# Kernel tuning notes

Measured on AMD Instinct MI355X. Metric: run time of the kernel, lower is better.

## Reference

```python
import jax, jax.numpy as jnp
import numpy as np
import math

GAUSSIAN_KERNEL = 3.0  # sigma from init_kwargs


def setup_inputs() -> dict:
    key = jax.random.key(0)
    k1, k2, k3, k4 = jax.random.split(key, 4)
    B, De, Do, T, H, W = 4, 128, 512, 10, 32, 32
    return {
        "m_in": jax.random.normal(k1, (B, De, T, H, W), dtype=jnp.float32),
        "m_out": jax.random.normal(k2, (B, Do, T, H, W), dtype=jnp.float32),
        "q_in": jax.random.normal(k3, (B, De, H, W), dtype=jnp.float32),
        "q_out": jax.random.normal(k4, (B, Do, H, W), dtype=jnp.float32),
    }


def _gaussian_kernel_map(corr, H, W, sigma):
    # corr: [B, THW, HW]; for each memory location, gaussian centered at its
    # argmax query position over the HxW query grid.
    idx = jnp.argmax(corr, axis=2)                       # [B, THW] int
    idx_y = (idx // W).astype(corr.dtype)[..., None, None]  # [B, THW, 1, 1]
    idx_x = (idx % W).astype(corr.dtype)[..., None, None]
    y = jnp.arange(H, dtype=corr.dtype).reshape(1, 1, H, 1)
    x = jnp.arange(W, dtype=corr.dtype).reshape(1, 1, 1, W)
    g = jnp.exp(-((x - idx_x) ** 2 + (y - idx_y) ** 2) / (2.0 * sigma ** 2))
    return g.reshape(corr.shape)                         # [B, THW, HW]


def reference(m_in, m_out, q_in, q_out):
    B, De, T, H, W = m_in.shape
    Do = m_out.shape[1]
    THW, HW = T * H * W, H * W

    mi = m_in.reshape(B, De, THW)       # [B, De, THW]
    qi = q_in.reshape(B, De, HW)        # [B, De, HW]
    # p[b, t, q] = <memory key t, query key q> / sqrt(De)
    p = jnp.einsum('bdt,bdq->btq', mi, qi) / math.sqrt(De)   # [B, THW, HW]

    gauss = _gaussian_kernel_map(p, H, W, GAUSSIAN_KERNEL)

    # softmax over memory dimension (dim=1), then gaussian reweight + renorm
    p_soft = jax.nn.softmax(p, axis=1)
    p_w = p_soft * gauss
    p_w = p_w / jnp.sum(p_w, axis=1, keepdims=True)

    mo = m_out.reshape(B, Do, THW)
    mem = jnp.einsum('bdt,btq->bdq', mo, p_w).reshape(B, Do, H, W)
    mem_out = jnp.concatenate([mem, q_out], axis=1)      # [B, 2*Do, H, W]
    return mem_out, p_w
```

## Files before the change

### kernel.cpp

```cpp
#include <hip/hip_runtime.h>
#include <hip/hip_bf16.h>

#define BB 4
#define DE 128
#define DO_ 512
#define THW 10240
#define HW 1024
#define SCALE 0.08838834764831845f
#define INV2S2 0.05555555555555555f
#define NCH 32
#define CHT 320

#define WS_PART_F  81920
#define WS_STATS_F 344064
#define WS_MO16_B  1409024ull
#define WS_PWT_B   43352064ull

using bf16x8 = __attribute__((ext_vector_type(8))) short;
using f32x4  = __attribute__((ext_vector_type(4))) float;
using u16x8  = __attribute__((ext_vector_type(8))) unsigned short;

__device__ __forceinline__ unsigned short f2bf(float f) {
    __hip_bfloat16 h = __float2bfloat16(f);
    return *reinterpret_cast<unsigned short*>(&h);
}
__device__ __forceinline__ void glds16(const void* g, void* l) {
    __builtin_amdgcn_global_load_lds((const __attribute__((address_space(1))) void*)g,
                                     (__attribute__((address_space(3))) void*)l,
                                     16, 0, 0);
}
__device__ __forceinline__ unsigned int ordf(float f) {
    unsigned int u = __float_as_uint(f);
    return (u & 0x80000000u) ? ~u : (u | 0x80000000u);
}

__global__ __launch_bounds__(256) void k_init(float* __restrict__ out,
                                              const float* __restrict__ qout,
                                              float4* __restrict__ amax4)
{
    int idx = blockIdx.x * 256 + threadIdx.x;
    if (idx < 20480) amax4[idx] = make_float4(0.f, 0.f, 0.f, 0.f);
    int b  = idx >> 18;
    int r  = idx & 262143;
    int c  = r >> 8;
    int q4 = r & 255;
    float4* dst = (float4*)out + idx;
    if (c < DO_) {
        *dst = make_float4(0.f, 0.f, 0.f, 0.f);
    } else {
        const float4* src = (const float4*)qout + ((size_t)(b * DO_ + (c - DO_)) << 8) + q4;
        *dst = *src;
    }
}

__global__ __launch_bounds__(256) void k_gemm1(const float* __restrict__ mi,
                                               const float* __restrict__ qi,
                                               float* __restrict__ p,
                                               unsigned long long* __restrict__ amax)
{
    __shared__ float As[32][128];
    __shared__ float Bs[32][128];
    int id  = blockIdx.x;
    int tbg = id & 7;
    int rr  = id >> 3;
    int b   = rr / 80;
    int j   = rr - b * 80;
    int tb  = tbg * 10 + (j >> 3);
    int qb  = j & 7;
    int tid = threadIdx.x;
    int tx = tid & 15, ty = tid >> 4;
    int lane = tid & 63;

    const float* A  = mi + (size_t)b * DE * THW + (size_t)tb * 128;
    const float* Bq = qi + (size_t)b * DE * HW  + qb * 128;

    float acc[8][8] = {};
    for (int kc = 0; kc < 4; ++kc) {
        __syncthreads();
#pragma unroll
        for (int i = 0; i < 4; ++i) {
            int s  = tid + i * 256;
            int kl = s >> 5;
            int c4 = (s & 31) << 2;
            *(float4*)&As[kl][c4] = *(const float4*)&A [(size_t)(kc * 32 + kl) * THW + c4];
            *(float4*)&Bs[kl][c4] = *(const float4*)&Bq[(size_t)(kc * 32 + kl) * HW  + c4];
        }
        __syncthreads();
#pragma unroll 2
        for (int kl = 0; kl < 32; ++kl) {
            float4 a0 = *(float4*)&As[kl][ty * 8];
            float4 a1 = *(float4*)&As[kl][ty * 8 + 4];
            float4 b0 = *(float4*)&Bs[kl][tx * 8];
            float4 b1 = *(float4*)&Bs[kl][tx * 8 + 4];
            float av[8] = {a0.x, a0.y, a0.z, a0.w, a1.x, a1.y, a1.z, a1.w};
            float bv[8] = {b0.x, b0.y, b0.z, b0.w, b1.x, b1.y, b1.z, b1.w};
#pragma unroll
            for (int i2 = 0; i2 < 8; ++i2)
#pragma unroll
                for (int j2 = 0; j2 < 8; ++j2)
                    acc[i2][j2] = fmaf(av[i2], bv[j2], acc[i2][j2]);
        }
    }

    size_t rowbase = ((size_t)b * THW + (size_t)tb * 128 + ty * 8) * HW + qb * 128 + tx * 8;
    int q0 = qb * 128 + tx * 8;
#pragma unroll
    for (int i = 0; i < 8; ++i) {
        float v[8];
#pragma unroll
        for (int j2 = 0; j2 < 8; ++j2) v[j2] = acc[i][j2] * SCALE;
        *(float4*)&p[rowbase + (size_t)i * HW]     = make_float4(v[0], v[1], v[2], v[3]);
        *(float4*)&p[rowbase + (size_t)i * HW + 4] = make_float4(v[4], v[5], v[6], v[7]);
        float best = v[0]; int bq = q0;
#pragma unroll
        for (int j2 = 1; j2 < 8; ++j2)
            if (v[j2] > best) { best = v[j2]; bq = q0 + j2; }
        unsigned long long pk = ((unsigned long long)ordf(best) << 32)
                              | (unsigned long long)(0xFFFFFFFFu - (unsigned)bq);
#pragma unroll
        for (int off = 1; off < 16; off <<= 1) {
            unsigned long long o = __shfl_xor(pk, off);
            if (o > pk) pk = o;
        }
        if ((lane & 15) == 0)
            atomicMax(&amax[(size_t)b * THW + (size_t)tb * 128 + ty * 8 + i], pk);
    }
}

__global__ __launch_bounds__(256) void k_colstats(const float* __restrict__ p,
                                                  const unsigned long long* __restrict__ amax,
                                                  float* __restrict__ part)
{
    int q  = blockIdx.x * 256 + threadIdx.x;
    int ch = blockIdx.y, b = blockIdx.z;
    float x = (float)(q & 31), y = (float)(q >> 5);
    const float* pp = p + ((size_t)b * THW + ch * CHT) * HW + q;
    const unsigned long long* am = amax + (size_t)b * THW + ch * CHT;
    float m = -3.0e38f, s = 0.f;
    for (int i = 0; i < CHT; ++i) {
        unsigned idx = 0xFFFFFFFFu - (unsigned)am[i];
        float dx = x - (float)(idx & 31), dy = y - (float)(idx >> 5);
        float z = pp[(size_t)i * HW] - (dx * dx + dy * dy) * INV2S2;
        float nm = fmaxf(m, z);
        s = s * __expf(m - nm) + __expf(z - nm);
        m = nm;
    }
    size_t o = ((size_t)(b * NCH + ch) * HW + q) * 2;
    part[o] = m; part[o + 1] = s;
}

__global__ __launch_bounds__(256) void k_reduce(const float* __restrict__ part,
                                                float* __restrict__ stats)
{
    int i = blockIdx.x * 256 + threadIdx.x;
    int b = i >> 10, q = i & 1023;
    float M = -3.0e38f;
#pragma unroll
    for (int c = 0; c < NCH; ++c)
        M = fmaxf(M, part[((size_t)(b * NCH + c) * HW + q) * 2]);
    float S = 0.f;
#pragma unroll
    for (int c = 0; c < NCH; ++c) {
        size_t o = ((size_t)(b * NCH + c) * HW + q) * 2;
        S += part[o + 1] * __expf(part[o] - M);
    }
    stats[(size_t)i * 2] = M;
    stats[(size_t)i * 2 + 1] = 1.0f / S;
}

__global__ __launch_bounds__(256) void k_pwt(float* __restrict__ p,
                                             const unsigned long long* __restrict__ amax,
                                             const float* __restrict__ stats,
                                             unsigned short* __restrict__ pwT)
{
    __shared__ float tile[64][65];
    __shared__ float ctr[128];
    __shared__ float st[128];
    int qb = blockIdx.x, tb = blockIdx.y, b = blockIdx.z;
    int tid = threadIdx.x;
    if (tid < 64) {
        unsigned idx = 0xFFFFFFFFu - (unsigned)amax[(size_t)b * THW + tb * 64 + tid];
        ctr[tid * 2]     = (float)(idx & 31);
        ctr[tid * 2 + 1] = (float)(idx >> 5);
    }
    if (tid < 128)
        st[tid] = stats[((size_t)b * HW + qb * 64) * 2 + tid];
    __syncthreads();
    int r0 = tid >> 4;
    int c4 = (tid & 15) << 2;
#pragma unroll
    for (int i = 0; i < 4; ++i) {
        int r = r0 + i * 16;
        float* pp = p + ((size_t)b * THW + tb * 64 + r) * HW + qb * 64 + c4;
        float4 v = *(float4*)pp;
        float cx = ctr[r * 2], cy = ctr[r * 2 + 1];
        float vv[4] = {v.x, v.y, v.z, v.w};
#pragma unroll
        for (int j = 0; j < 4; ++j) {
            int q = qb * 64 + c4 + j;
            float x = (float)(q & 31), y = (float)(q >> 5);
            float dx = x - cx, dy = y - cy;
            vv[j] = __expf(vv[j] - (dx * dx + dy * dy) * INV2S2 - st[(c4 + j) * 2])
                    * st[(c4 + j) * 2 + 1];
            tile[r][c4 + j] = vv[j];
        }
        *(float4*)pp = make_float4(vv[0], vv[1], vv[2], vv[3]);
    }
    __syncthreads();
    int ql = tid >> 3;
    int t0 = (tid & 7) << 3;
#pragma unroll
    for (int pass = 0; pass < 2; ++pass) {
        int q = ql + pass * 32;
        u16x8 o8;
#pragma unroll
        for (int j = 0; j < 8; ++j)
            o8[j] = f2bf(tile[t0 + j][q]);
        *(u16x8*)&pwT[((size_t)b * HW + qb * 64 + q) * THW + tb * 64 + t0] = o8;
    }
}

__global__ __launch_bounds__(256) void k_mo16(const float* __restrict__ mo,
                                              unsigned short* __restrict__ o)
{
    size_t base = ((size_t)blockIdx.x * 256 + threadIdx.x) * 8;
    float4 a = *(const float4*)(mo + base);
    float4 c = *(const float4*)(mo + base + 4);
    u16x8 v;
    v[0] = f2bf(a.x); v[1] = f2bf(a.y); v[2] = f2bf(a.z); v[3] = f2bf(a.w);
    v[4] = f2bf(c.x); v[5] = f2bf(c.y); v[6] = f2bf(c.z); v[7] = f2bf(c.w);
    *(u16x8*)(o + base) = v;
}

__global__ __launch_bounds__(256) void k_gemm2m(const unsigned short* __restrict__ A16,
                                                const unsigned short* __restrict__ B16,
                                                float* __restrict__ out)
{
    __shared__ unsigned short As[4096];
    __shared__ unsigned short Bs[4096];
    int id   = blockIdx.x;
    int xcd  = id & 7;
    int rest = id >> 3;
    int shi  = rest >> 5;
    int jj   = rest & 31;
    int s    = xcd + (shi << 3);
    int b    = s >> 2, ks = s & 3;
    int mb   = jj >> 3, nb = jj & 7;
    int tid = threadIdx.x;
    int w = tid >> 6, lane = tid & 63;
    int quad = lane >> 4, l15 = lane & 15;

    const char* Ag = (const char*)(A16 + (size_t)b * DO_ * THW + (size_t)mb * 128 * THW + ks * 2560);
    const char* Bg = (const char*)(B16 + (size_t)b * HW * THW + (size_t)nb * 128 * THW + ks * 2560);

    int srow = lane >> 2;
    int sj   = (lane & 3) ^ (srow & 3);
    const char* aP0 = Ag + (size_t)((w * 2 + 0) * 16 + srow) * (THW * 2) + sj * 16;
    const char* aP1 = Ag + (size_t)((w * 2 + 1) * 16 + srow) * (THW * 2) + sj * 16;
    const char* bP0 = Bg + (size_t)((w * 2 + 0) * 16 + srow) * (THW * 2) + sj * 16;
    const char* bP1 = Bg + (size_t)((w * 2 + 1) * 16 + srow) * (THW * 2) + sj * 16;
    char* lA0 = (char*)As + (w * 2 + 0) * 1024;
    char* lA1 = (char*)As + (w * 2 + 1) * 1024;
    char* lB0 = (char*)Bs + (w * 2 + 0) * 1024;
    char* lB1 = (char*)Bs + (w * 2 + 1) * 1024;

    int wm = w >> 1, wn = w & 1;
    int fq = ((l15 & 3) ^ quad) << 4;
    const char* aF = (const char*)As + (wm * 64 + l15) * 64 + fq;
    const char* bF = (const char*)Bs + (wn * 64 + l15) * 64 + fq;

    f32x4 acc[4][4];
#pragma unroll
    for (int i = 0; i < 4; ++i)
#pragma unroll
        for (int j = 0; j < 4; ++j)
            acc[i][j] = (f32x4){0.f, 0.f, 0.f, 0.f};

    for (int kit = 0; kit < 80; ++kit) {
        int kb = kit * 64;
        __syncthreads();
        glds16(aP0 + kb, lA0);
        glds16(aP1 + kb, lA1);
        glds16(bP0 + kb, lB0);
        glds16(bP1 + kb, lB1);
        __syncthreads();
        bf16x8 af[4], bfr[4];
#pragma unroll
        for (int i = 0; i < 4; ++i) af[i]  = *(const bf16x8*)(aF + i * 1024);
#pragma unroll
        for (int j = 0; j < 4; ++j) bfr[j] = *(const bf16x8*)(bF + j * 1024);
#pragma unroll
        for (int i = 0; i < 4; ++i)
#pragma unroll
            for (int j = 0; j < 4; ++j)
                acc[i][j] = __builtin_amdgcn_mfma_f32_16x16x32_bf16(af[i], bfr[j], acc[i][j], 0, 0, 0);
    }

    float* Cg = out + (size_t)b * (2 * DO_ * HW);
    int d0 = mb * 128 + wm * 64 + quad * 4;
    int q0 = nb * 128 + wn * 64 + l15;
#pragma unroll
    for (int i = 0; i < 4; ++i)
#pragma unroll
        for (int j = 0; j < 4; ++j)
#pragma unroll
            for (int r = 0; r < 4; ++r)
                atomicAdd(&Cg[(size_t)(d0 + i * 16 + r) * HW + q0 + j * 16], acc[i][j][r]);
}

extern "C" void kernel_launch(void* const* d_in, const int* in_sizes, int n_in,
                              void* d_out, int out_size, void* d_ws, size_t ws_size,
                              hipStream_t stream)
{
    const float* m_in  = (const float*)d_in[0];
    const float* m_out = (const float*)d_in[1];
    const float* q_in  = (const float*)d_in[2];
    const float* q_out = (const float*)d_in[3];
    float* out = (float*)d_out;
    float* pw  = out + (size_t)BB * 2 * DO_ * HW;
    float* ws  = (float*)d_ws;
    unsigned long long* amax = (unsigned long long*)d_ws;
    float* part    = ws + WS_PART_F;
    float* stats   = ws + WS_STATS_F;
    unsigned short* mo16  = (unsigned short*)((char*)d_ws + WS_MO16_B);
    unsigned short* pwT16 = (unsigned short*)((char*)d_ws + WS_PWT_B);

    hipLaunchKernelGGL(k_init,    dim3(4096),        dim3(256), 0, stream, out, q_out, (float4*)d_ws);
    hipLaunchKernelGGL(k_mo16,    dim3(10240),       dim3(256), 0, stream, m_out, mo16);
    hipLaunchKernelGGL(k_gemm1,   dim3(2560),        dim3(256), 0, stream, m_in, q_in, pw, amax);
    hipLaunchKernelGGL(k_colstats,dim3(4, NCH, BB),  dim3(256), 0, stream, pw, amax, part);
    hipLaunchKernelGGL(k_reduce,  dim3(16),          dim3(256), 0, stream, part, stats);
    hipLaunchKernelGGL(k_pwt,     dim3(16, 160, BB), dim3(256), 0, stream, pw, amax, stats, pwT16);
    hipLaunchKernelGGL(k_gemm2m,  dim3(512),         dim3(256), 0, stream, mo16, pwT16, out);
}
```

Measured before the change: 576.4 us.

## Run first GEMM on fp16 MFMA with hi/lo split for fp32 accuracy

Replaces the scalar fp32 FMA GEMM for the key correlation with an MFMA fp16 GEMM. The inputs are first split into high and low fp16 parts, transposed to a K-contiguous layout, and the query scale is folded in. Three MFMA products (HH, HL, LH) approximate fp32 accuracy, and LDS is filled with global_load_lds and XOR swizzling. The split buffers reuse the pwT16 workspace region, so the mo16 conversion launch is moved after the stats kernels. The cost is extra conversion passes and some precision risk near argmax ties.

```diff
diff --git a/kernel.cpp b/kernel.cpp
--- a/kernel.cpp
+++ b/kernel.cpp
@@ -15,8 +15,13 @@
 #define WS_STATS_F 344064
 #define WS_MO16_B  1409024ull
 #define WS_PWT_B   43352064ull
+#define WS_MITH_B  (WS_PWT_B)
+#define WS_MITL_B  (WS_PWT_B + 10485760ull)
+#define WS_QITH_B  (WS_PWT_B + 20971520ull)
+#define WS_QITL_B  (WS_PWT_B + 22020096ull)
 
 using bf16x8 = __attribute__((ext_vector_type(8))) short;
+using f16x8  = __attribute__((ext_vector_type(8))) _Float16;
 using f32x4  = __attribute__((ext_vector_type(4))) float;
 using u16x8  = __attribute__((ext_vector_type(8))) unsigned short;
 
@@ -53,13 +58,56 @@
     }
 }
 
-__global__ __launch_bounds__(256) void k_gemm1(const float* __restrict__ mi,
-                                               const float* __restrict__ qi,
-                                               float* __restrict__ p,
-                                               unsigned long long* __restrict__ amax)
-{
-    __shared__ float As[32][128];
-    __shared__ float Bs[32][128];
+__global__ __launch_bounds__(256) void k_split(const float* __restrict__ src,
+                                               unsigned short* __restrict__ dstH,
+                                               unsigned short* __restrict__ dstL,
+                                               int ncols, float scale)
+{
+    __shared__ float tile[128][65];
+    int t0 = blockIdx.x * 64;
+    int b  = blockIdx.z;
+    int tid = threadIdx.x;
+    const float* S = src + (size_t)b * DE * ncols + t0;
+#pragma unroll
+    for (int i = 0; i < 8; ++i) {
+        int s  = tid + i * 256;
+        int k  = s >> 4;
+        int c4 = (s & 15) << 2;
+        *(float4*)&tile[k][c4] = *(const float4*)&S[(size_t)k * ncols + c4];
+    }
+    __syncthreads();
+#pragma unroll
+    for (int i = 0; i < 4; ++i) {
+        int s  = tid + i * 256;
+        int t  = s >> 4;
+        int k8 = s & 15;
+        u16x8 oh, ol;
+#pragma unroll
+        for (int j = 0; j < 8; ++j) {
+            float v = tile[k8 * 8 + j][t] * scale;
+            _Float16 h = (_Float16)v;
+            float rr = v - (float)h;
+            _Float16 l = (_Float16)(rr * 2048.0f);
+            oh[j] = *(unsigned short*)&h;
+            ol[j] = *(unsigned short*)&l;
+        }
+        size_t o = ((size_t)b * ncols + t0 + t) * 128 + k8 * 8;
+        *(u16x8*)&dstH[o] = oh;
+        *(u16x8*)&dstL[o] = ol;
+    }
+}
+
+__global__ __launch_bounds__(256) void k_gemm1m(const unsigned short* __restrict__ AH,
+                                                const unsigned short* __restrict__ AL,
+                                                const unsigned short* __restrict__ BH,
+                                                const unsigned short* __restrict__ BL,
+                                                float* __restrict__ p,
+                                                unsigned long long* __restrict__ amax)
+{
+    __shared__ unsigned short AsH[4096];
+    __shared__ unsigned short AsL[4096];
+    __shared__ unsigned short BsH[4096];
+    __shared__ unsigned short BsL[4096];
     int id  = blockIdx.x;
     int tbg = id & 7;
     int rr  = id >> 3;
@@ -68,62 +116,102 @@
     int tb  = tbg * 10 + (j >> 3);
     int qb  = j & 7;
     int tid = threadIdx.x;
-    int tx = tid & 15, ty = tid >> 4;
-    int lane = tid & 63;
-
-    const float* A  = mi + (size_t)b * DE * THW + (size_t)tb * 128;
-    const float* Bq = qi + (size_t)b * DE * HW  + qb * 128;
-
-    float acc[8][8] = {};
+    int w = tid >> 6, lane = tid & 63;
+    int quad = lane >> 4, l15 = lane & 15;
+
+    const char* AgH = (const char*)AH + ((size_t)b * THW + (size_t)tb * 128) * 256;
+    const char* AgL = (const char*)AL + ((size_t)b * THW + (size_t)tb * 128) * 256;
+    const char* BgH = (const char*)BH + ((size_t)b * HW + qb * 128) * 256;
+    const char* BgL = (const char*)BL + ((size_t)b * HW + qb * 128) * 256;
+
+    int srow = lane >> 2;
+    int sj   = (lane & 3) ^ (srow & 3);
+    size_t ro0 = (size_t)(w * 32 + srow) * 256 + sj * 16;
+    size_t ro1 = (size_t)(w * 32 + 16 + srow) * 256 + sj * 16;
+    char* lds0[4] = {(char*)AsH + w * 2048, (char*)AsL + w * 2048,
+                     (char*)BsH + w * 2048, (char*)BsL + w * 2048};
+    const char* gl0[4] = {AgH, AgL, BgH, BgL};
+
+    int wm = w >> 1, wn = w & 1;
+    int fq = ((l15 & 3) ^ quad) << 4;
+    const char* aFH = (const char*)AsH + (wm * 64 + l15) * 64 + fq;
+    const char* aFL = (const char*)AsL + (wm * 64 + l15) * 64 + fq;
+    const char* bFH = (const char*)BsH + (wn * 64 + l15) * 64 + fq;
+    const char* bFL = (const char*)BsL + (wn * 64 + l15) * 64 + fq;
+
+    f32x4 acc1[4][4], acc2[4][4];
+#pragma unroll
+    for (int i = 0; i < 4; ++i)
+#pragma unroll
+        for (int j2 = 0; j2 < 4; ++j2) {
+            acc1[i][j2] = (f32x4){0.f, 0.f, 0.f, 0.f};
+            acc2[i][j2] = (f32x4){0.f, 0.f, 0.f, 0.f};
+        }
+
     for (int kc = 0; kc < 4; ++kc) {
+        size_t kb = (size_t)kc * 64;
         __syncthreads();
 #pragma unroll
+        for (int m = 0; m < 4; ++m) {
+            glds16(gl0[m] + ro0 + kb, lds0[m]);
+            glds16(gl0[m] + ro1 + kb, lds0[m] + 1024);
+        }
+        __syncthreads();
+        f16x8 afH[4], afL[4], bfH[4], bfL[4];
+#pragma unroll
         for (int i = 0; i < 4; ++i) {
-            int s  = tid + i * 256;
-            int kl = s >> 5;
-            int c4 = (s & 31) << 2;
-            *(float4*)&As[kl][c4] = *(const float4*)&A [(size_t)(kc * 32 + kl) * THW + c4];
-            *(float4*)&Bs[kl][c4] = *(const float4*)&Bq[(size_t)(kc * 32 + kl) * HW  + c4];
-        }
-        __syncthreads();
-#pragma unroll 2
-        for (int kl = 0; kl < 32; ++kl) {
-            float4 a0 = *(float4*)&As[kl][ty * 8];
-            float4 a1 = *(float4*)&As[kl][ty * 8 + 4];
-            float4 b0 = *(float4*)&Bs[kl][tx * 8];
-            float4 b1 = *(float4*)&Bs[kl][tx * 8 + 4];
-            float av[8] = {a0.x, a0.y, a0.z, a0.w, a1.x, a1.y, a1.z, a1.w};
-            float bv[8] = {b0.x, b0.y, b0.z, b0.w, b1.x, b1.y, b1.z, b1.w};
-#pragma unroll
-            for (int i2 = 0; i2 < 8; ++i2)
-#pragma unroll
-                for (int j2 = 0; j2 < 8; ++j2)
-                    acc[i2][j2] = fmaf(av[i2], bv[j2], acc[i2][j2]);
-        }
-    }
-
-    size_t rowbase = ((size_t)b * THW + (size_t)tb * 128 + ty * 8) * HW + qb * 128 + tx * 8;
-    int q0 = qb * 128 + tx * 8;
-#pragma unroll
-    for (int i = 0; i < 8; ++i) {
-        float v[8];
-#pragma unroll
-        for (int j2 = 0; j2 < 8; ++j2) v[j2] = acc[i][j2] * SCALE;
-        *(float4*)&p[rowbase + (size_t)i * HW]     = make_float4(v[0], v[1], v[2], v[3]);
-        *(float4*)&p[rowbase + (size_t)i * HW + 4] = make_float4(v[4], v[5], v[6], v[7]);
-        float best = v[0]; int bq = q0;
-#pragma unroll
-        for (int j2 = 1; j2 < 8; ++j2)
-            if (v[j2] > best) { best = v[j2]; bq = q0 + j2; }
-        unsigned long long pk = ((unsigned long long)ordf(best) << 32)
-                              | (unsigned long long)(0xFFFFFFFFu - (unsigned)bq);
-#pragma unroll
-        for (int off = 1; off < 16; off <<= 1) {
-            unsigned long long o = __shfl_xor(pk, off);
-            if (o > pk) pk = o;
-        }
-        if ((lane & 15) == 0)
-            atomicMax(&amax[(size_t)b * THW + (size_t)tb * 128 + ty * 8 + i], pk);
+            afH[i] = *(const f16x8*)(aFH + i * 1024);
+            afL[i] = *(const f16x8*)(aFL + i * 1024);
+            bfH[i] = *(const f16x8*)(bFH + i * 1024);
+            bfL[i] = *(const f16x8*)(bFL + i * 1024);
+        }
+#pragma unroll
+        for (int i = 0; i < 4; ++i)
+#pragma unroll
+            for (int j2 = 0; j2 < 4; ++j2)
+                acc1[i][j2] = __builtin_amdgcn_mfma_f32_16x16x32_f16(afH[i], bfH[j2], acc1[i][j2], 0, 0, 0);
+#pragma unroll
+        for (int i = 0; i < 4; ++i)
+#pragma unroll
+            for (int j2 = 0; j2 < 4; ++j2)
+                acc2[i][j2] = __builtin_amdgcn_mfma_f32_16x16x32_f16(afH[i], bfL[j2], acc2[i][j2], 0, 0, 0);
+#pragma unroll
+        for (int i = 0; i < 4; ++i)
+#pragma unroll
+            for (int j2 = 0; j2 < 4; ++j2)
+                acc2[i][j2] = __builtin_amdgcn_mfma_f32_16x16x32_f16(afL[i], bfH[j2], acc2[i][j2], 0, 0, 0);
+    }
+
+    const float inv2048 = 4.8828125e-4f;
+    int t0 = tb * 128 + wm * 64;
+    float* Pg = p + ((size_t)b * THW + t0) * HW + qb * 128 + wn * 64;
+    int qbase = qb * 128 + wn * 64;
+#pragma unroll
+    for (int i = 0; i < 4; ++i) {
+#pragma unroll
+        for (int r = 0; r < 4; ++r) {
+            int tl = i * 16 + quad * 4 + r;
+            float v[4];
+#pragma unroll
+            for (int j2 = 0; j2 < 4; ++j2) {
+                v[j2] = acc1[i][j2][r] + acc2[i][j2][r] * inv2048;
+                Pg[(size_t)tl * HW + j2 * 16 + l15] = v[j2];
+            }
+            float best = v[0]; int bj = 0;
+#pragma unroll
+            for (int j2 = 1; j2 < 4; ++j2)
+                if (v[j2] > best) { best = v[j2]; bj = j2; }
+            int q = qbase + bj * 16 + l15;
+            unsigned long long pk = ((unsigned long long)ordf(best) << 32)
+                                  | (unsigned long long)(0xFFFFFFFFu - (unsigned)q);
+#pragma unroll
+            for (int off = 1; off < 16; off <<= 1) {
+                unsigned long long o = __shfl_xor(pk, off);
+                if (o > pk) pk = o;
+            }
+            if (l15 == 0)
+                atomicMax(&amax[(size_t)b * THW + t0 + tl], pk);
+        }
     }
 }
 
@@ -324,12 +412,18 @@
     float* stats   = ws + WS_STATS_F;
     unsigned short* mo16  = (unsigned short*)((char*)d_ws + WS_MO16_B);
     unsigned short* pwT16 = (unsigned short*)((char*)d_ws + WS_PWT_B);
+    unsigned short* miTH  = (unsigned short*)((char*)d_ws + WS_MITH_B);
+    unsigned short* miTL  = (unsigned short*)((char*)d_ws + WS_MITL_B);
+    unsigned short* qiTH  = (unsigned short*)((char*)d_ws + WS_QITH_B);
+    unsigned short* qiTL  = (unsigned short*)((char*)d_ws + WS_QITL_B);
 
     hipLaunchKernelGGL(k_init,    dim3(4096),        dim3(256), 0, stream, out, q_out, (float4*)d_ws);
-    hipLaunchKernelGGL(k_mo16,    dim3(10240),       dim3(256), 0, stream, m_out, mo16);
-    hipLaunchKernelGGL(k_gemm1,   dim3(2560),        dim3(256), 0, stream, m_in, q_in, pw, amax);
+    hipLaunchKernelGGL(k_split,   dim3(160, 1, BB),  dim3(256), 0, stream, m_in, miTH, miTL, THW, 1.0f);
+    hipLaunchKernelGGL(k_split,   dim3(16, 1, BB),   dim3(256), 0, stream, q_in, qiTH, qiTL, HW, SCALE);
+    hipLaunchKernelGGL(k_gemm1m,  dim3(2560),        dim3(256), 0, stream, miTH, miTL, qiTH, qiTL, pw, amax);
     hipLaunchKernelGGL(k_colstats,dim3(4, NCH, BB),  dim3(256), 0, stream, pw, amax, part);
     hipLaunchKernelGGL(k_reduce,  dim3(16),          dim3(256), 0, stream, part, stats);
+    hipLaunchKernelGGL(k_mo16,    dim3(10240),       dim3(256), 0, stream, m_out, mo16);
     hipLaunchKernelGGL(k_pwt,     dim3(16, 160, BB), dim3(256), 0, stream, pw, amax, stats, pwT16);
     hipLaunchKernelGGL(k_gemm2m,  dim3(512),         dim3(256), 0, stream, mo16, pwT16, out);
 }
```

Measured after the change: 516.8 us. 10.3% less time.
